# Optimization experiments

Measured on AMD Instinct MI355X. Metric: run time of the kernel, lower is better.

## Reference

```python
import jax, jax.numpy as jnp
import numpy as np

EPSILON = 0.1      # init kwarg epsilon
NUM_STAB = 1e-06   # init kwarg num_stab
B, D, C = 4096, 3072, 10


def setup_inputs() -> dict:
    key = jax.random.key(0)
    k1, k2 = jax.random.split(key)
    data = jax.random.normal(k1, (B, D), dtype=jnp.float32)
    # small scale keeps softmax probs near-uniform -> rho well-conditioned
    W = jax.random.normal(k2, (D, C), dtype=jnp.float32) * 0.02
    return {"data": data, "W": W}


def _probs(logits, c):
    # output = softmax(...) * (1 - c*num_stab) + num_stab  (numerical stabilization)
    p = jax.nn.softmax(logits, axis=-1)
    return p * (1.0 - c * NUM_STAB) + NUM_STAB


def reference(data, W):
    c = W.shape[1]
    m = c - 1

    def g(x):  # x: [D] -> new_output row: [m]
        p = _probs(x @ W, c)
        s = jnp.sqrt(p)
        return 2.0 * s[:m] / (1.0 - s[m])

    # Vectorized Jacobian: replaces the m sequential autograd.grad calls.
    jac = jax.vmap(jax.jacrev(g))(data)            # [B, m, D]

    p = _probs(data @ W, c)                        # [B, C]
    s_m = jnp.sqrt(p[:, m])                        # [B]
    delta = 2.0 * jnp.arccos(jnp.sqrt(p / c).sum(axis=1))   # [B]
    rho = (2.0 * (1.0 - s_m) - p[:, :m].sum(axis=1)) / (1.0 - s_m)  # [B]
    jac_norm = jnp.sqrt(jnp.square(jac).sum(axis=(1, 2)))   # [B] Frobenius norm per sample
    reg = jax.nn.elu(jac_norm - delta / (rho * EPSILON))
    return reg.mean()
```

## Files before the change

### kernel.cpp

```cpp
#include <hip/hip_runtime.h>
#include <math.h>

#define NB 4096
#define ND 3072
#define NC 10
#define NM 9

static constexpr float kEps      = 0.1f;
static constexpr float kNumStab  = 1e-6f;
static constexpr float kAlpha    = 1.0f - (float)NC * kNumStab;
static constexpr float kInvSqrtC = 0.31622776601683794f;

__global__ __launch_bounds__(256) void transpose_kernel(
        const float* __restrict__ W, float* __restrict__ Wt) {
    const int c = blockIdx.x * 256 + threadIdx.x;
    if (c >= (NC * ND) / 4) return;
    const int k = c / (ND / 4);
    const int m = c - k * (ND / 4);
    float4 v;
    v.x = W[(4 * m + 0) * NC + k];
    v.y = W[(4 * m + 1) * NC + k];
    v.z = W[(4 * m + 2) * NC + k];
    v.w = W[(4 * m + 3) * NC + k];
    reinterpret_cast<float4*>(Wt)[c] = v;
}

__global__ __launch_bounds__(256) void gram_kernel(
        const float* __restrict__ Wt, float* __restrict__ G) {
    const int j = blockIdx.x / NC;
    const int k = blockIdx.x % NC;
    const float4* a = reinterpret_cast<const float4*>(Wt + j * ND);
    const float4* b = reinterpret_cast<const float4*>(Wt + k * ND);
    float acc = 0.0f;
    for (int i = threadIdx.x; i < ND / 4; i += 256) {
        const float4 av = a[i], bv = b[i];
        acc += av.x * bv.x + av.y * bv.y + av.z * bv.z + av.w * bv.w;
    }
    #pragma unroll
    for (int off = 32; off > 0; off >>= 1) acc += __shfl_xor(acc, off, 64);
    __shared__ float part[4];
    if ((threadIdx.x & 63) == 0) part[threadIdx.x >> 6] = acc;
    __syncthreads();
    if (threadIdx.x == 0) G[blockIdx.x] = part[0] + part[1] + part[2] + part[3];
}

__global__ __launch_bounds__(1024, 4) void jacreg_kernel(
        const float* __restrict__ data, const float* __restrict__ Wt,
        const float* __restrict__ G, float* __restrict__ out) {
    __shared__ float Wts[NC * ND];
    __shared__ float Gs[100];
    __shared__ float pzs[16][24];
    __shared__ float regs[16];

    const int tid  = threadIdx.x;
    const int lane = tid & 63;
    const int wv   = tid >> 6;
    const int q    = wv >> 1;
    const int half = wv & 1;

    if (tid < 100) Gs[tid] = G[tid];

    const int s0 = blockIdx.x * 16 + q * 2;
    const float* __restrict__ r0 = data + (size_t)s0 * ND + half * (ND / 2);
    const float* __restrict__ r1 = r0 + ND;

    float4 x0 = reinterpret_cast<const float4*>(r0)[lane];
    float4 x1 = reinterpret_cast<const float4*>(r1)[lane];

    {
        const float4* src = reinterpret_cast<const float4*>(Wt);
        float4* dst = reinterpret_cast<float4*>(Wts);
        #pragma unroll
        for (int i = 0; i < 8; ++i) {
            const int c = tid + i * 1024;
            if (c < (NC * ND) / 4) dst[c] = src[c];
        }
    }
    __syncthreads();

    float acc[2][NC];
    #pragma unroll
    for (int s = 0; s < 2; ++s)
        #pragma unroll
        for (int k = 0; k < NC; ++k) acc[s][k] = 0.0f;

    const int dbase0 = half * (ND / 2);
    #pragma unroll
    for (int it = 0; it < 6; ++it) {
        const int nit = (it == 5) ? 5 : it + 1;
        const float4 nx0 = reinterpret_cast<const float4*>(r0)[nit * 64 + lane];
        const float4 nx1 = reinterpret_cast<const float4*>(r1)[nit * 64 + lane];

        const int dbase = dbase0 + it * 256 + lane * 4;
        #pragma unroll
        for (int k = 0; k < NC; ++k) {
            const float4 wt = *reinterpret_cast<const float4*>(&Wts[k * ND + dbase]);
            acc[0][k] = fmaf(x0.x, wt.x, acc[0][k]);
            acc[0][k] = fmaf(x0.y, wt.y, acc[0][k]);
            acc[0][k] = fmaf(x0.z, wt.z, acc[0][k]);
            acc[0][k] = fmaf(x0.w, wt.w, acc[0][k]);
            acc[1][k] = fmaf(x1.x, wt.x, acc[1][k]);
            acc[1][k] = fmaf(x1.y, wt.y, acc[1][k]);
            acc[1][k] = fmaf(x1.z, wt.z, acc[1][k]);
            acc[1][k] = fmaf(x1.w, wt.w, acc[1][k]);
        }
        x0 = nx0;
        x1 = nx1;
    }

    #pragma unroll
    for (int s = 0; s < 2; ++s)
        #pragma unroll
        for (int k = 0; k < NC; ++k) {
            float v = acc[s][k];
            #pragma unroll
            for (int off = 32; off > 0; off >>= 1) v += __shfl_xor(v, off, 64);
            acc[s][k] = v;
        }

    if (lane == 0) {
        float4* p = reinterpret_cast<float4*>(&pzs[wv][0]);
        p[0] = make_float4(acc[0][0], acc[0][1], acc[0][2], acc[0][3]);
        p[1] = make_float4(acc[0][4], acc[0][5], acc[0][6], acc[0][7]);
        p[2] = make_float4(acc[0][8], acc[0][9], 0.0f, 0.0f);
        p[3] = make_float4(acc[1][0], acc[1][1], acc[1][2], acc[1][3]);
        p[4] = make_float4(acc[1][4], acc[1][5], acc[1][6], acc[1][7]);
        p[5] = make_float4(acc[1][8], acc[1][9], 0.0f, 0.0f);
    }
    __syncthreads();

    if (half == 0 && lane < 2) {
        float z[NC];
        #pragma unroll
        for (int k = 0; k < NC; ++k)
            z[k] = pzs[wv][lane * 12 + k] + pzs[wv + 1][lane * 12 + k];

        float zm = z[0];
        #pragma unroll
        for (int k = 1; k < NC; ++k) zm = fmaxf(zm, z[k]);
        float e[NC], Zs = 0.0f;
        #pragma unroll
        for (int k = 0; k < NC; ++k) { e[k] = expf(z[k] - zm); Zs += e[k]; }
        const float inv = 1.0f / Zs;

        float sg[NC], p[NC], sq[NC], u[NC];
        #pragma unroll
        for (int k = 0; k < NC; ++k) {
            sg[k] = e[k] * inv;
            p[k]  = kAlpha * sg[k] + kNumStab;
            sq[k] = sqrtf(p[k]);
            u[k]  = sg[k] / sq[k];
        }
        const float qd = 1.0f - sq[NM];

        float v[NC], t = 0.0f;
        #pragma unroll
        for (int k = 0; k < NC; ++k) {
            float a = 0.0f;
            #pragma unroll
            for (int j = 0; j < NC; ++j) a = fmaf(Gs[k * NC + j], sg[j], a);
            v[k] = a;
            t = fmaf(sg[k], a, t);
        }
        const float vM = v[NM], uM = u[NM];
        const float QMM = Gs[NC * NC - 1] - 2.0f * vM + t;

        float sumJ = 0.0f;
        #pragma unroll
        for (int i = 0; i < NM; ++i) {
            const float Qii = Gs[i * NC + i] - 2.0f * v[i] + t;
            const float QiM = Gs[i * NC + NM] - v[i] - vM + t;
            const float r = sq[i] / qd;
            sumJ += u[i] * u[i] * Qii
                  + 2.0f * u[i] * uM * r * QiM
                  + uM * uM * r * r * QMM;
        }
        const float jn = (kAlpha / qd) * sqrtf(fmaxf(sumJ, 0.0f));

        float ssum = 0.0f;
        #pragma unroll
        for (int k = 0; k < NC; ++k) ssum += sq[k];
        const float ac = fminf(1.0f, fmaxf(-1.0f, ssum * kInvSqrtC));
        const float delta = 2.0f * acosf(ac);

        float psum = 0.0f;
        #pragma unroll
        for (int k = 0; k < NM; ++k) psum += p[k];
        const float rho = (2.0f * qd - psum) / qd;

        const float a = jn - delta / (rho * kEps);
        regs[q * 2 + lane] = (a > 0.0f) ? a : expm1f(a);
    }
    __syncthreads();
    if (tid == 0) {
        float bs = 0.0f;
        #pragma unroll
        for (int i = 0; i < 16; ++i) bs += regs[i];
        atomicAdd(out, bs * (1.0f / (float)NB));
    }
}

extern "C" void kernel_launch(void* const* d_in, const int* in_sizes, int n_in,
                              void* d_out, int out_size, void* d_ws, size_t ws_size,
                              hipStream_t stream) {
    const float* data = (const float*)d_in[0];
    const float* W    = (const float*)d_in[1];
    float* out = (float*)d_out;
    float* Wt  = (float*)d_ws;
    float* G   = Wt + NC * ND;

    hipMemsetAsync(out, 0, sizeof(float), stream);
    transpose_kernel<<<(NC * ND / 4 + 255) / 256, 256, 0, stream>>>(W, Wt);
    gram_kernel<<<NC * NC, 256, 0, stream>>>(Wt, G);
    jacreg_kernel<<<NB / 16, 1024, 0, stream>>>(data, Wt, G, out);
}
```

Measured before the change: 107.2 us.

## Fuse transpose and Gram computation into main kernel, deepen data prefetch

Drops the separate transpose and Gram kernels. Each block now transposes W straight into padded shared memory, with the stride set to avoid bank conflicts, and computes the 10x10 Gram matrix itself. This removes two kernel launches and their serial dependency, at the cost of every block repeating the Gram work and doing scattered shared-memory writes during the transpose. Data prefetch is also deepened to two iterations ahead. Gs is read later only after an existing __syncthreads, so correctness holds.

```diff
diff --git a/kernel.cpp b/kernel.cpp
--- a/kernel.cpp
+++ b/kernel.cpp
@@ -5,50 +5,18 @@
 #define ND 3072
 #define NC 10
 #define NM 9
+#define WSTRIDE 3076
 
 static constexpr float kEps      = 0.1f;
 static constexpr float kNumStab  = 1e-6f;
 static constexpr float kAlpha    = 1.0f - (float)NC * kNumStab;
 static constexpr float kInvSqrtC = 0.31622776601683794f;
 
-__global__ __launch_bounds__(256) void transpose_kernel(
-        const float* __restrict__ W, float* __restrict__ Wt) {
-    const int c = blockIdx.x * 256 + threadIdx.x;
-    if (c >= (NC * ND) / 4) return;
-    const int k = c / (ND / 4);
-    const int m = c - k * (ND / 4);
-    float4 v;
-    v.x = W[(4 * m + 0) * NC + k];
-    v.y = W[(4 * m + 1) * NC + k];
-    v.z = W[(4 * m + 2) * NC + k];
-    v.w = W[(4 * m + 3) * NC + k];
-    reinterpret_cast<float4*>(Wt)[c] = v;
-}
-
-__global__ __launch_bounds__(256) void gram_kernel(
-        const float* __restrict__ Wt, float* __restrict__ G) {
-    const int j = blockIdx.x / NC;
-    const int k = blockIdx.x % NC;
-    const float4* a = reinterpret_cast<const float4*>(Wt + j * ND);
-    const float4* b = reinterpret_cast<const float4*>(Wt + k * ND);
-    float acc = 0.0f;
-    for (int i = threadIdx.x; i < ND / 4; i += 256) {
-        const float4 av = a[i], bv = b[i];
-        acc += av.x * bv.x + av.y * bv.y + av.z * bv.z + av.w * bv.w;
-    }
-    #pragma unroll
-    for (int off = 32; off > 0; off >>= 1) acc += __shfl_xor(acc, off, 64);
-    __shared__ float part[4];
-    if ((threadIdx.x & 63) == 0) part[threadIdx.x >> 6] = acc;
-    __syncthreads();
-    if (threadIdx.x == 0) G[blockIdx.x] = part[0] + part[1] + part[2] + part[3];
-}
-
-__global__ __launch_bounds__(1024, 4) void jacreg_kernel(
-        const float* __restrict__ data, const float* __restrict__ Wt,
-        const float* __restrict__ G, float* __restrict__ out) {
-    __shared__ float Wts[NC * ND];
-    __shared__ float Gs[100];
+__global__ __launch_bounds__(1024) void fused_kernel(
+        const float* __restrict__ data, const float* __restrict__ W,
+        float* __restrict__ out) {
+    __shared__ float Wts[NC * WSTRIDE];
+    __shared__ float Gs[112];
     __shared__ float pzs[16][24];
     __shared__ float regs[16];
 
@@ -58,26 +26,54 @@
     const int q    = wv >> 1;
     const int half = wv & 1;
 
-    if (tid < 100) Gs[tid] = G[tid];
-
     const int s0 = blockIdx.x * 16 + q * 2;
     const float* __restrict__ r0 = data + (size_t)s0 * ND + half * (ND / 2);
     const float* __restrict__ r1 = r0 + ND;
 
-    float4 x0 = reinterpret_cast<const float4*>(r0)[lane];
-    float4 x1 = reinterpret_cast<const float4*>(r1)[lane];
+    float4 xa0 = reinterpret_cast<const float4*>(r0)[lane];
+    float4 xa1 = reinterpret_cast<const float4*>(r1)[lane];
+    float4 xb0 = reinterpret_cast<const float4*>(r0)[64 + lane];
+    float4 xb1 = reinterpret_cast<const float4*>(r1)[64 + lane];
 
     {
-        const float4* src = reinterpret_cast<const float4*>(Wt);
-        float4* dst = reinterpret_cast<float4*>(Wts);
+        const float4* W4 = reinterpret_cast<const float4*>(W);
         #pragma unroll
         for (int i = 0; i < 8; ++i) {
             const int c = tid + i * 1024;
-            if (c < (NC * ND) / 4) dst[c] = src[c];
+            if (c < (ND * NC) / 4) {
+                const float4 w4 = W4[c];
+                const float* wp = reinterpret_cast<const float*>(&w4);
+                const int e0 = c * 4;
+                #pragma unroll
+                for (int j = 0; j < 4; ++j) {
+                    const int e = e0 + j;
+                    Wts[(e % NC) * WSTRIDE + (e / NC)] = wp[j];
+                }
+            }
         }
     }
     __syncthreads();
 
+    #pragma unroll
+    for (int n = 0; n < 7; ++n) {
+        const int e = wv * 7 + n;
+        if (e < NC * NC) {
+            const int gj = e / NC, gk = e % NC;
+            float a = 0.0f;
+            #pragma unroll
+            for (int c = 0; c < 12; ++c) {
+                const float4 aj = *reinterpret_cast<const float4*>(
+                    &Wts[gj * WSTRIDE + c * 256 + lane * 4]);
+                const float4 bk = *reinterpret_cast<const float4*>(
+                    &Wts[gk * WSTRIDE + c * 256 + lane * 4]);
+                a += aj.x * bk.x + aj.y * bk.y + aj.z * bk.z + aj.w * bk.w;
+            }
+            #pragma unroll
+            for (int off = 32; off > 0; off >>= 1) a += __shfl_xor(a, off, 64);
+            if (lane == 0) Gs[e] = a;
+        }
+    }
+
     float acc[2][NC];
     #pragma unroll
     for (int s = 0; s < 2; ++s)
@@ -87,25 +83,27 @@
     const int dbase0 = half * (ND / 2);
     #pragma unroll
     for (int it = 0; it < 6; ++it) {
-        const int nit = (it == 5) ? 5 : it + 1;
-        const float4 nx0 = reinterpret_cast<const float4*>(r0)[nit * 64 + lane];
-        const float4 nx1 = reinterpret_cast<const float4*>(r1)[nit * 64 + lane];
+        float4 xc0 = xb0, xc1 = xb1;
+        if (it < 4) {
+            xc0 = reinterpret_cast<const float4*>(r0)[(it + 2) * 64 + lane];
+            xc1 = reinterpret_cast<const float4*>(r1)[(it + 2) * 64 + lane];
+        }
 
         const int dbase = dbase0 + it * 256 + lane * 4;
         #pragma unroll
         for (int k = 0; k < NC; ++k) {
-            const float4 wt = *reinterpret_cast<const float4*>(&Wts[k * ND + dbase]);
-            acc[0][k] = fmaf(x0.x, wt.x, acc[0][k]);
-            acc[0][k] = fmaf(x0.y, wt.y, acc[0][k]);
-            acc[0][k] = fmaf(x0.z, wt.z, acc[0][k]);
-            acc[0][k] = fmaf(x0.w, wt.w, acc[0][k]);
-            acc[1][k] = fmaf(x1.x, wt.x, acc[1][k]);
-            acc[1][k] = fmaf(x1.y, wt.y, acc[1][k]);
-            acc[1][k] = fmaf(x1.z, wt.z, acc[1][k]);
-            acc[1][k] = fmaf(x1.w, wt.w, acc[1][k]);
-        }
-        x0 = nx0;
-        x1 = nx1;
+            const float4 wt = *reinterpret_cast<const float4*>(&Wts[k * WSTRIDE + dbase]);
+            acc[0][k] = fmaf(xa0.x, wt.x, acc[0][k]);
+            acc[0][k] = fmaf(xa0.y, wt.y, acc[0][k]);
+            acc[0][k] = fmaf(xa0.z, wt.z, acc[0][k]);
+            acc[0][k] = fmaf(xa0.w, wt.w, acc[0][k]);
+            acc[1][k] = fmaf(xa1.x, wt.x, acc[1][k]);
+            acc[1][k] = fmaf(xa1.y, wt.y, acc[1][k]);
+            acc[1][k] = fmaf(xa1.z, wt.z, acc[1][k]);
+            acc[1][k] = fmaf(xa1.w, wt.w, acc[1][k]);
+        }
+        xa0 = xb0; xa1 = xb1;
+        xb0 = xc0; xb1 = xc1;
     }
 
     #pragma unroll
@@ -206,11 +204,7 @@
     const float* data = (const float*)d_in[0];
     const float* W    = (const float*)d_in[1];
     float* out = (float*)d_out;
-    float* Wt  = (float*)d_ws;
-    float* G   = Wt + NC * ND;
 
     hipMemsetAsync(out, 0, sizeof(float), stream);
-    transpose_kernel<<<(NC * ND / 4 + 255) / 256, 256, 0, stream>>>(W, Wt);
-    gram_kernel<<<NC * NC, 256, 0, stream>>>(Wt, G);
-    jacreg_kernel<<<NB / 16, 1024, 0, stream>>>(data, Wt, G, out);
+    fused_kernel<<<NB / 16, 1024, 0, stream>>>(data, W, out);
 }
```

Result: no change. 106.7 us (-0.5%).

## Drop transpose and LDS staging; read W directly with one wave per sample

Applied to the files above, without the earlier changes.

Removes the transpose kernel and the per-block copy of the full 120KB transposed W into shared memory. Each wave now computes one sample's logits by reading the original row-major W with contiguous float4 loads, relying on L2/L1 caching. The Gram kernel computes only the upper triangle and mirrors it. This frees LDS so more blocks can be resident, at the cost of every wave re-reading W from cache and not reusing it across two samples.

```diff
diff --git a/kernel.cpp b/kernel.cpp
--- a/kernel.cpp
+++ b/kernel.cpp
@@ -11,129 +11,79 @@
 static constexpr float kAlpha    = 1.0f - (float)NC * kNumStab;
 static constexpr float kInvSqrtC = 0.31622776601683794f;
 
-__global__ __launch_bounds__(256) void transpose_kernel(
-        const float* __restrict__ W, float* __restrict__ Wt) {
-    const int c = blockIdx.x * 256 + threadIdx.x;
-    if (c >= (NC * ND) / 4) return;
-    const int k = c / (ND / 4);
-    const int m = c - k * (ND / 4);
-    float4 v;
-    v.x = W[(4 * m + 0) * NC + k];
-    v.y = W[(4 * m + 1) * NC + k];
-    v.z = W[(4 * m + 2) * NC + k];
-    v.w = W[(4 * m + 3) * NC + k];
-    reinterpret_cast<float4*>(Wt)[c] = v;
-}
 
 __global__ __launch_bounds__(256) void gram_kernel(
-        const float* __restrict__ Wt, float* __restrict__ G) {
-    const int j = blockIdx.x / NC;
-    const int k = blockIdx.x % NC;
-    const float4* a = reinterpret_cast<const float4*>(Wt + j * ND);
-    const float4* b = reinterpret_cast<const float4*>(Wt + k * ND);
+        const float* __restrict__ W, float* __restrict__ G) {
+    int e = blockIdx.x, j = 0;
+    while (e >= NC - j) { e -= NC - j; ++j; }
+    const int k = j + e;
     float acc = 0.0f;
-    for (int i = threadIdx.x; i < ND / 4; i += 256) {
-        const float4 av = a[i], bv = b[i];
-        acc += av.x * bv.x + av.y * bv.y + av.z * bv.z + av.w * bv.w;
-    }
+    for (int d = threadIdx.x; d < ND; d += 256)
+        acc = fmaf(W[d * NC + j], W[d * NC + k], acc);
     #pragma unroll
     for (int off = 32; off > 0; off >>= 1) acc += __shfl_xor(acc, off, 64);
     __shared__ float part[4];
     if ((threadIdx.x & 63) == 0) part[threadIdx.x >> 6] = acc;
     __syncthreads();
-    if (threadIdx.x == 0) G[blockIdx.x] = part[0] + part[1] + part[2] + part[3];
+    if (threadIdx.x == 0) {
+        const float g = part[0] + part[1] + part[2] + part[3];
+        G[j * NC + k] = g;
+        G[k * NC + j] = g;
+    }
 }
 
-__global__ __launch_bounds__(1024, 4) void jacreg_kernel(
-        const float* __restrict__ data, const float* __restrict__ Wt,
+__global__ __launch_bounds__(256, 4) void main_kernel(
+        const float* __restrict__ data, const float* __restrict__ W,
         const float* __restrict__ G, float* __restrict__ out) {
-    __shared__ float Wts[NC * ND];
     __shared__ float Gs[100];
-    __shared__ float pzs[16][24];
-    __shared__ float regs[16];
+    __shared__ float regs[4];
 
     const int tid  = threadIdx.x;
     const int lane = tid & 63;
     const int wv   = tid >> 6;
-    const int q    = wv >> 1;
-    const int half = wv & 1;
 
     if (tid < 100) Gs[tid] = G[tid];
-
-    const int s0 = blockIdx.x * 16 + q * 2;
-    const float* __restrict__ r0 = data + (size_t)s0 * ND + half * (ND / 2);
-    const float* __restrict__ r1 = r0 + ND;
-
-    float4 x0 = reinterpret_cast<const float4*>(r0)[lane];
-    float4 x1 = reinterpret_cast<const float4*>(r1)[lane];
-
-    {
-        const float4* src = reinterpret_cast<const float4*>(Wt);
-        float4* dst = reinterpret_cast<float4*>(Wts);
-        #pragma unroll
-        for (int i = 0; i < 8; ++i) {
-            const int c = tid + i * 1024;
-            if (c < (NC * ND) / 4) dst[c] = src[c];
-        }
-    }
     __syncthreads();
 
-    float acc[2][NC];
+    const int s = blockIdx.x * 4 + wv;
+    const float4* d4 = reinterpret_cast<const float4*>(data) + (size_t)s * (ND / 4);
+    const float4* W4 = reinterpret_cast<const float4*>(W);
+
+    float acc[NC];
     #pragma unroll
-    for (int s = 0; s < 2; ++s)
+    for (int k = 0; k < NC; ++k) acc[k] = 0.0f;
+
+    #pragma unroll 2
+    for (int it = 0; it < 12; ++it) {
+        const int f = it * 64 + lane;
+        const float4 x = d4[f];
+        const float4* wp = W4 + (size_t)f * 10;
+        float4 wq[10];
         #pragma unroll
-        for (int k = 0; k < NC; ++k) acc[s][k] = 0.0f;
-
-    const int dbase0 = half * (ND / 2);
-    #pragma unroll
-    for (int it = 0; it < 6; ++it) {
-        const int nit = (it == 5) ? 5 : it + 1;
-        const float4 nx0 = reinterpret_cast<const float4*>(r0)[nit * 64 + lane];
-        const float4 nx1 = reinterpret_cast<const float4*>(r1)[nit * 64 + lane];
-
-        const int dbase = dbase0 + it * 256 + lane * 4;
+        for (int jj = 0; jj < 10; ++jj) wq[jj] = wp[jj];
+        const float xs[4] = {x.x, x.y, x.z, x.w};
         #pragma unroll
-        for (int k = 0; k < NC; ++k) {
-            const float4 wt = *reinterpret_cast<const float4*>(&Wts[k * ND + dbase]);
-            acc[0][k] = fmaf(x0.x, wt.x, acc[0][k]);
-            acc[0][k] = fmaf(x0.y, wt.y, acc[0][k]);
-            acc[0][k] = fmaf(x0.z, wt.z, acc[0][k]);
-            acc[0][k] = fmaf(x0.w, wt.w, acc[0][k]);
-            acc[1][k] = fmaf(x1.x, wt.x, acc[1][k]);
-            acc[1][k] = fmaf(x1.y, wt.y, acc[1][k]);
-            acc[1][k] = fmaf(x1.z, wt.z, acc[1][k]);
-            acc[1][k] = fmaf(x1.w, wt.w, acc[1][k]);
+        for (int jj = 0; jj < 10; ++jj) {
+            const int mb = 4 * jj;
+            acc[(mb + 0) % 10] = fmaf(xs[(mb + 0) / 10], wq[jj].x, acc[(mb + 0) % 10]);
+            acc[(mb + 1) % 10] = fmaf(xs[(mb + 1) / 10], wq[jj].y, acc[(mb + 1) % 10]);
+            acc[(mb + 2) % 10] = fmaf(xs[(mb + 2) / 10], wq[jj].z, acc[(mb + 2) % 10]);
+            acc[(mb + 3) % 10] = fmaf(xs[(mb + 3) / 10], wq[jj].w, acc[(mb + 3) % 10]);
         }
-        x0 = nx0;
-        x1 = nx1;
     }
 
     #pragma unroll
-    for (int s = 0; s < 2; ++s)
+    for (int k = 0; k < NC; ++k) {
+        float v = acc[k];
         #pragma unroll
-        for (int k = 0; k < NC; ++k) {
-            float v = acc[s][k];
-            #pragma unroll
-            for (int off = 32; off > 0; off >>= 1) v += __shfl_xor(v, off, 64);
-            acc[s][k] = v;
-        }
+        for (int off = 32; off > 0; off >>= 1) v += __shfl_xor(v, off, 64);
+        acc[k] = v;
+    }
 
     if (lane == 0) {
-        float4* p = reinterpret_cast<float4*>(&pzs[wv][0]);
-        p[0] = make_float4(acc[0][0], acc[0][1], acc[0][2], acc[0][3]);
-        p[1] = make_float4(acc[0][4], acc[0][5], acc[0][6], acc[0][7]);
-        p[2] = make_float4(acc[0][8], acc[0][9], 0.0f, 0.0f);
-        p[3] = make_float4(acc[1][0], acc[1][1], acc[1][2], acc[1][3]);
-        p[4] = make_float4(acc[1][4], acc[1][5], acc[1][6], acc[1][7]);
-        p[5] = make_float4(acc[1][8], acc[1][9], 0.0f, 0.0f);
-    }
-    __syncthreads();
-
-    if (half == 0 && lane < 2) {
         float z[NC];
         #pragma unroll
-        for (int k = 0; k < NC; ++k)
-            z[k] = pzs[wv][lane * 12 + k] + pzs[wv + 1][lane * 12 + k];
+        for (int k = 0; k < NC; ++k) z[k] = acc[k];
 
         float zm = z[0];
         #pragma unroll
@@ -189,14 +139,11 @@
         const float rho = (2.0f * qd - psum) / qd;
 
         const float a = jn - delta / (rho * kEps);
-        regs[q * 2 + lane] = (a > 0.0f) ? a : expm1f(a);
+        regs[wv] = (a > 0.0f) ? a : expm1f(a);
     }
     __syncthreads();
     if (tid == 0) {
-        float bs = 0.0f;
-        #pragma unroll
-        for (int i = 0; i < 16; ++i) bs += regs[i];
-        atomicAdd(out, bs * (1.0f / (float)NB));
+        atomicAdd(out, (regs[0] + regs[1] + regs[2] + regs[3]) * (1.0f / (float)NB));
     }
 }
 
@@ -206,11 +153,9 @@
     const float* data = (const float*)d_in[0];
     const float* W    = (const float*)d_in[1];
     float* out = (float*)d_out;
-    float* Wt  = (float*)d_ws;
-    float* G   = Wt + NC * ND;
+    float* G   = (float*)d_ws;
 
     hipMemsetAsync(out, 0, sizeof(float), stream);
-    transpose_kernel<<<(NC * ND / 4 + 255) / 256, 256, 0, stream>>>(W, Wt);
-    gram_kernel<<<NC * NC, 256, 0, stream>>>(Wt, G);
-    jacreg_kernel<<<NB / 16, 1024, 0, stream>>>(data, Wt, G, out);
+    gram_kernel<<<(NC * (NC + 1)) / 2, 256, 0, stream>>>(W, G);
+    main_kernel<<<NB / 4, 256, 0, stream>>>(data, W, G, out);
 }
```

Result: slower. 115.9 us (+8.1%).
